# Kernel optimization log

Hardware: AMD Instinct MI355X
Metric: run time of the kernel (lower is better)

The kernel has to match this reference:

```python
import jax, jax.numpy as jnp
import numpy as np
import math

B, S, P, G = 8, 512, 64, 64
E, GE = 768, 32          # sub_embed_dim, gene_embed_dim
HD = E // 2              # sub_head_dim = 384
L = P * G
LAMBDA_INIT = 0.8 - 0.6 * math.exp(-0.3 * 0)  # depth=0 -> 0.2
SCALING = HD ** -0.5


def setup_inputs() -> dict:
    key0 = jax.random.key(0)
    ks = jax.random.split(key0, 12)
    init = 0.02
    return {
        "query": jax.random.normal(ks[0], (B, S, E), jnp.float32),
        "key": jax.random.normal(ks[1], (B, P, G, GE), jnp.float32),
        "query_mask": jax.random.bernoulli(ks[2], 0.9, (B, S)),
        "key_mask": jax.random.bernoulli(ks[3], 0.9, (B, P, G)),
        # weights stored [in, out] so y = x @ W (equiv to torch Linear no-bias)
        "Wq": jax.random.normal(ks[4], (E, E), jnp.float32) * init,
        "Wkv": jax.random.normal(ks[5], (GE, 2 * E), jnp.float32) * init,
        "Wout": jax.random.normal(ks[6], (E, E), jnp.float32) * init,
        "lambda_q1": jax.random.normal(ks[7], (HD,), jnp.float32) * 0.1,
        "lambda_k1": jax.random.normal(ks[8], (HD,), jnp.float32) * 0.1,
        "lambda_q2": jax.random.normal(ks[9], (HD,), jnp.float32) * 0.1,
        "lambda_k2": jax.random.normal(ks[10], (HD,), jnp.float32) * 0.1,
        "ln_weight": jnp.ones((E,), jnp.float32),  # RMSNorm affine weight (2*HD = E)
    }


def reference(query, key, query_mask, key_mask, Wq, Wkv, Wout,
              lambda_q1, lambda_k1, lambda_q2, lambda_k2, ln_weight):
    # Projections
    Q = query @ Wq                                   # [B,S,E]
    KV = key.reshape(B, L, GE) @ Wkv                 # [B,L,2E]
    K = KV[..., :E]                                  # [B,L,E]
    V = KV[..., E:]                                  # [B,L,E] (= 2*HD)

    # Split into 2 heads of dim HD
    Qh = Q.reshape(B, S, 2, HD).transpose(0, 2, 1, 3) * SCALING   # [B,2,S,HD]
    Kh = K.reshape(B, L, 2, HD).transpose(0, 2, 1, 3)             # [B,2,L,HD]

    # Combined mask [B,S,L]
    mask = query_mask[:, :, None] & key_mask.reshape(B, L)[:, None, :]

    # Dual attention scores + stable softmax (eps=1e-8 on denominator)
    scores = jnp.einsum('bhsd,bhld->bhsl', Qh, Kh)                # [B,2,S,L]
    scores = jnp.where(mask[:, None], scores, -1e20)
    m = jnp.max(scores, axis=-1, keepdims=True)
    p = jnp.exp(scores - m)
    attn = p / (jnp.sum(p, axis=-1, keepdims=True) + 1e-8)

    # Differential combination
    lam = (jnp.exp(jnp.sum(lambda_q1 * lambda_k1))
           - jnp.exp(jnp.sum(lambda_q2 * lambda_k2)) + LAMBDA_INIT)
    diff = attn[:, 0] - lam * attn[:, 1]                          # [B,S,L]
    diff = diff - jnp.min(diff, axis=-1, keepdims=True) + 1e-20
    diff = jnp.where(mask, diff, 0.0)

    # Value contraction: [B,S,L] @ [B,L,E] -> [B,S,E]
    attn_out = jnp.einsum('bsl,ble->bse', diff, V)

    # RMSNorm (eps=1e-5, affine) then scale by (1 - lambda_init)
    ms = jnp.mean(attn_out * attn_out, axis=-1, keepdims=True)
    attn_out = attn_out * jax.lax.rsqrt(ms + 1e-5) * ln_weight
    attn_out = attn_out * (1.0 - LAMBDA_INIT)

    out = attn_out @ Wout                                         # [B,S,E]
    return out, diff.reshape(B, S, P, G)
```

## Files before the change

kernel.cpp:

```cpp
#include <hip/hip_runtime.h>
#include <math.h>

#define LAM_INIT 0.2f
#define ONE_MINUS_LAM 0.8f
#define SCALING_F 0.05103103630798288f

typedef _Float16 h2 __attribute__((ext_vector_type(2)));

#if defined(__has_builtin)
#if __has_builtin(__builtin_amdgcn_fdot2)
#define FDOT2(a, b, c) __builtin_amdgcn_fdot2((a), (b), (c), false)
#endif
#endif
#ifndef FDOT2
#define FDOT2(a, b, c) ((float)(a).x * (float)(b).x + ((float)(a).y * (float)(b).y + (c)))
#endif

__device__ inline float waveMin(float v) {
#pragma unroll
    for (int o = 32; o > 0; o >>= 1) v = fminf(v, __shfl_xor(v, o));
    return v;
}
__device__ inline float waveSum(float v) {
#pragma unroll
    for (int o = 32; o > 0; o >>= 1) v += __shfl_xor(v, o);
    return v;
}

__global__ __launch_bounds__(256) void k01_prep(
    const float* __restrict__ key, const float* __restrict__ Wq,
    const float* __restrict__ Wkv, const float* __restrict__ Wout,
    const float* __restrict__ lq1, const float* __restrict__ lk1,
    const float* __restrict__ lq2, const float* __restrict__ lk2,
    const float* __restrict__ ln,
    unsigned* __restrict__ keyThU, float* __restrict__ Wcp,
    float* __restrict__ Wvp, float* __restrict__ lam,
    float* __restrict__ M)
{
    int blk = blockIdx.x;
    int tid = threadIdx.x;
    if (blk < 128) {
        int b  = blk >> 4;
        int l0 = (blk & 15) << 8;
        __shared__ float tile[256 * 33];
        const float* kp = key + ((size_t)b * 4096 + l0) * 32;
#pragma unroll
        for (int q = 0; q < 32; ++q) {
            int idx = tid + (q << 8);
            int r = idx >> 5, g = idx & 31;
            tile[r * 33 + g] = kp[idx];
        }
        __syncthreads();
#pragma unroll
        for (int gp = 0; gp < 16; ++gp) {
            h2 v;
            v.x = (_Float16)tile[tid * 33 + 2 * gp];
            v.y = (_Float16)tile[tid * 33 + 2 * gp + 1];
            keyThU[((size_t)(b * 16 + gp)) * 4096 + l0 + tid] =
                __builtin_bit_cast(unsigned, v);
        }
    } else if (blk < 512) {
        int bb = blk - 128;
        int kc = bb & 1;
        int ob = bb >> 1;
        int idx = ob * 256 + tid;
        int e  = idx >> 6;
        int hg = idx & 63;
        int h = hg >> 5, g = hg & 31;
        const float4* wqr = (const float4*)(Wq  + (size_t)e * 768 + h * 384 + kc * 192);
        const float4* wkr = (const float4*)(Wkv + (size_t)g * 1536 + h * 384 + kc * 192);
        float s0 = 0.f, s1 = 0.f;
#pragma unroll 4
        for (int d = 0; d < 48; d += 2) {
            float4 a0 = wqr[d],   b0 = wkr[d];
            float4 a1 = wqr[d+1], b1 = wkr[d+1];
            s0 += a0.x*b0.x + a0.y*b0.y + a0.z*b0.z + a0.w*b0.w;
            s1 += a1.x*b1.x + a1.y*b1.y + a1.z*b1.z + a1.w*b1.w;
        }
        Wcp[kc * 49152 + idx] = (s0 + s1) * SCALING_F;
    } else if (blk < 1280) {
        int bb = blk - 512;
        int kc = bb / 96;
        int ob = bb - kc * 96;
        int idx = ob * 256 + tid;
        int g = idx / 768;
        int e = idx - g * 768;
        const float* wvr = Wkv + (size_t)g * 1536 + 768;
        int c0 = kc * 96;
        float s0 = 0.f, s1 = 0.f;
#pragma unroll 4
        for (int c = c0; c < c0 + 96; c += 2) {
            s0 += wvr[c]   * ln[c]   * Wout[(size_t)c * 768 + e];
            s1 += wvr[c+1] * ln[c+1] * Wout[(size_t)(c+1) * 768 + e];
        }
        Wvp[kc * 24576 + idx] = s0 + s1;
    } else if (blk == 1280) {
        float s1 = 0.f, s2 = 0.f;
        for (int d = tid; d < 384; d += 256) {
            s1 += lq1[d] * lk1[d];
            s2 += lq2[d] * lk2[d];
        }
        s1 = waveSum(s1);
        s2 = waveSum(s2);
        __shared__ float r1[4], r2[4];
        int wid = tid >> 6, lane = tid & 63;
        if (lane == 0) { r1[wid] = s1; r2[wid] = s2; }
        __syncthreads();
        if (tid == 0) {
            float a  = r1[0] + r1[1] + r1[2] + r1[3];
            float b2 = r2[0] + r2[1] + r2[2] + r2[3];
            lam[0] = expf(a) - expf(b2) + LAM_INIT;
        }
    } else {
        int idx = (blk - 1281) * 256 + tid;
        int g = idx >> 5, gp = idx & 31;
        const float4* ra = (const float4*)(Wkv + (size_t)g  * 1536 + 768);
        const float4* rb = (const float4*)(Wkv + (size_t)gp * 1536 + 768);
        float s = 0.f;
#pragma unroll 4
        for (int q = 0; q < 192; ++q) {
            float4 a = ra[q], b = rb[q];
            s += a.x*b.x + a.y*b.y + a.z*b.z + a.w*b.w;
        }
        M[idx] = s;
    }
}

__global__ __launch_bounds__(256) void k2_qt(
    const float* __restrict__ query, const float* __restrict__ Wcp,
    const float* __restrict__ Wvp, float* __restrict__ WvoT,
    float* __restrict__ Qtp)
{
    int blk = blockIdx.x;
    int tid = threadIdx.x;
    if (blk >= 512) {
        int idx = (blk - 512) * 256 + tid;
        float s = 0.f;
#pragma unroll
        for (int kc = 0; kc < 8; ++kc) s += Wvp[kc * 24576 + idx];
        int g = idx / 768;
        int e = idx - g * 768;
        WvoT[(size_t)e * 32 + g] = s;
        return;
    }
    int kc = blk >> 7;
    int mt = blk & 127;
    int m0 = mt * 32;
    __shared__ __align__(16) float As[64 * 33];
    __shared__ __align__(16) float Bs[64 * 64];

    int tm = tid >> 5;
    int tn = tid & 31;
    float acc[4][2];
#pragma unroll
    for (int r = 0; r < 4; ++r) { acc[r][0] = 0.f; acc[r][1] = 0.f; }

    for (int ch = 0; ch < 3; ++ch) {
        int k0 = kc * 192 + ch * 64;
        __syncthreads();
#pragma unroll
        for (int q = 0; q < 2; ++q) {
            int f = tid + q * 256;
            int m = f >> 4, kq = f & 15;
            float4 v = *(const float4*)&query[(size_t)(m0 + m) * 768 + k0 + kq * 4];
            As[(kq * 4 + 0) * 33 + m] = v.x;
            As[(kq * 4 + 1) * 33 + m] = v.y;
            As[(kq * 4 + 2) * 33 + m] = v.z;
            As[(kq * 4 + 3) * 33 + m] = v.w;
        }
#pragma unroll
        for (int q = 0; q < 4; ++q) {
            int f = tid + q * 256;
            int kk = f >> 4, n4 = f & 15;
            float4 a = *(const float4*)&Wcp[(size_t)(k0 + kk) * 64 + n4 * 4];
            float4 b = *(const float4*)&Wcp[49152 + (size_t)(k0 + kk) * 64 + n4 * 4];
            float4 s; s.x = a.x + b.x; s.y = a.y + b.y; s.z = a.z + b.z; s.w = a.w + b.w;
            *(float4*)&Bs[kk * 64 + n4 * 4] = s;
        }
        __syncthreads();
#pragma unroll 8
        for (int kk = 0; kk < 64; ++kk) {
            float4 a = *(const float4*)&As[kk * 33 + tm * 4];
            float2 b = *(const float2*)&Bs[kk * 64 + tn * 2];
            acc[0][0] += a.x * b.x; acc[0][1] += a.x * b.y;
            acc[1][0] += a.y * b.x; acc[1][1] += a.y * b.y;
            acc[2][0] += a.z * b.x; acc[2][1] += a.z * b.y;
            acc[3][0] += a.w * b.x; acc[3][1] += a.w * b.y;
        }
    }
#pragma unroll
    for (int r = 0; r < 4; ++r) {
        float2 o; o.x = acc[r][0]; o.y = acc[r][1];
        *(float2*)&Qtp[(size_t)kc * 262144 + (size_t)(m0 + tm * 4 + r) * 64 + tn * 2] = o;
    }
}

__global__ __launch_bounds__(512, 4) void k3_attn(
    const float* __restrict__ Qtp, const unsigned* __restrict__ keyThU,
    const int* __restrict__ qmask, const int* __restrict__ kmask,
    const float* __restrict__ lamp, float* __restrict__ diffO)
{
    int blk = blockIdx.x;
    int b  = blk >> 7;
    int s0 = (blk & 127) * 4;
    int tid = threadIdx.x;
    int lane = tid & 63, wid = tid >> 6;

    __shared__ __align__(16) unsigned qt_th[128];
    __shared__ float redS[64];
    __shared__ float redM[32];

    if (tid < 128) {
        int ts = tid >> 5;
        int h  = (tid >> 4) & 1;
        int gp = tid & 15;
        size_t row = (size_t)(b * 512 + s0 + ts) * 64;
        int col = h * 32 + 2 * gp;
        float v0 = 0.f, v1 = 0.f;
#pragma unroll
        for (int kc = 0; kc < 4; ++kc) {
            v0 += Qtp[(size_t)kc * 262144 + row + col];
            v1 += Qtp[(size_t)kc * 262144 + row + col + 1];
        }
        h2 hv; hv.x = (_Float16)v0; hv.y = (_Float16)v1;
        qt_th[gp * 8 + ts * 2 + h] = __builtin_bit_cast(unsigned, hv);
    }
    int qm[4];
#pragma unroll
    for (int ts = 0; ts < 4; ++ts) qm[ts] = qmask[b * 512 + s0 + ts];
    float lam = lamp[0];

    unsigned kmb = 0;
#pragma unroll
    for (int c = 0; c < 2; ++c) {
        int4 km = *(const int4*)(kmask + b * 4096 + c * 2048 + tid * 4);
        if (km.x) kmb |= 1u << (c * 4 + 0);
        if (km.y) kmb |= 1u << (c * 4 + 1);
        if (km.z) kmb |= 1u << (c * 4 + 2);
        if (km.w) kmb |= 1u << (c * 4 + 3);
    }
    __syncthreads();

    float p[2][4][8];
#pragma unroll
    for (int h = 0; h < 2; ++h)
#pragma unroll
        for (int ts = 0; ts < 4; ++ts)
#pragma unroll
            for (int i = 0; i < 8; ++i) p[h][ts][i] = 0.f;

    const unsigned* kt = keyThU + (size_t)b * 16 * 4096 + tid * 4;
    for (int gp = 0; gp < 16; ++gp) {
        uint4 q0 = *(const uint4*)&qt_th[gp * 8];
        uint4 q1 = *(const uint4*)&qt_th[gp * 8 + 4];
        h2 qv[8];
        qv[0] = __builtin_bit_cast(h2, q0.x); qv[1] = __builtin_bit_cast(h2, q0.y);
        qv[2] = __builtin_bit_cast(h2, q0.z); qv[3] = __builtin_bit_cast(h2, q0.w);
        qv[4] = __builtin_bit_cast(h2, q1.x); qv[5] = __builtin_bit_cast(h2, q1.y);
        qv[6] = __builtin_bit_cast(h2, q1.z); qv[7] = __builtin_bit_cast(h2, q1.w);
        const unsigned* kg = kt + (size_t)gp * 4096;
#pragma unroll
        for (int c = 0; c < 2; ++c) {
            uint4 kv = *(const uint4*)(kg + c * 2048);
            h2 k0 = __builtin_bit_cast(h2, kv.x);
            h2 k1 = __builtin_bit_cast(h2, kv.y);
            h2 k2 = __builtin_bit_cast(h2, kv.z);
            h2 k3 = __builtin_bit_cast(h2, kv.w);
#pragma unroll
            for (int ts = 0; ts < 4; ++ts)
#pragma unroll
                for (int h = 0; h < 2; ++h) {
                    h2 q = qv[ts * 2 + h];
                    p[h][ts][c*4+0] = FDOT2(k0, q, p[h][ts][c*4+0]);
                    p[h][ts][c*4+1] = FDOT2(k1, q, p[h][ts][c*4+1]);
                    p[h][ts][c*4+2] = FDOT2(k2, q, p[h][ts][c*4+2]);
                    p[h][ts][c*4+3] = FDOT2(k3, q, p[h][ts][c*4+3]);
                }
        }
    }

    float inv[2][4];
#pragma unroll
    for (int h = 0; h < 2; ++h)
#pragma unroll
        for (int ts = 0; ts < 4; ++ts) {
            float s = 0.f;
#pragma unroll
            for (int i = 0; i < 8; ++i) {
                bool ok = qm[ts] && ((kmb >> i) & 1u);
                float e = ok ? __expf(p[h][ts][i]) : 0.f;
                p[h][ts][i] = e;
                s += e;
            }
            s = waveSum(s);
            if (lane == 0) redS[(h * 4 + ts) * 8 + wid] = s;
        }
    __syncthreads();
#pragma unroll
    for (int h = 0; h < 2; ++h)
#pragma unroll
        for (int ts = 0; ts < 4; ++ts) {
            int r = (h * 4 + ts) * 8;
            float s = redS[r];
#pragma unroll
            for (int w = 1; w < 8; ++w) s += redS[r + w];
            inv[h][ts] = 1.0f / (s + 1e-8f);
        }

    float mn[4];
#pragma unroll
    for (int ts = 0; ts < 4; ++ts) {
        float v = 3.4e38f;
#pragma unroll
        for (int i = 0; i < 8; ++i) {
            float d = p[0][ts][i] * inv[0][ts] - lam * (p[1][ts][i] * inv[1][ts]);
            p[0][ts][i] = d;
            v = fminf(v, d);
        }
        v = waveMin(v);
        if (lane == 0) redM[ts * 8 + wid] = v;
    }
    __syncthreads();
#pragma unroll
    for (int ts = 0; ts < 4; ++ts) {
        int r = ts * 8;
        float v = redM[r];
#pragma unroll
        for (int w = 1; w < 8; ++w) v = fminf(v, redM[r + w]);
        mn[ts] = v;
    }

#pragma unroll
    for (int ts = 0; ts < 4; ++ts) {
        size_t base = (size_t)(b * 512 + s0 + ts) * 4096 + tid * 4;
#pragma unroll
        for (int c = 0; c < 2; ++c) {
            float4 o;
            float v0 = p[0][ts][c*4+0] - mn[ts] + 1e-20f;
            float v1 = p[0][ts][c*4+1] - mn[ts] + 1e-20f;
            float v2 = p[0][ts][c*4+2] - mn[ts] + 1e-20f;
            float v3 = p[0][ts][c*4+3] - mn[ts] + 1e-20f;
            o.x = (qm[ts] && ((kmb >> (c*4+0)) & 1u)) ? v0 : 0.f;
            o.y = (qm[ts] && ((kmb >> (c*4+1)) & 1u)) ? v1 : 0.f;
            o.z = (qm[ts] && ((kmb >> (c*4+2)) & 1u)) ? v2 : 0.f;
            o.w = (qm[ts] && ((kmb >> (c*4+3)) & 1u)) ? v3 : 0.f;
            *(float4*)(diffO + base + c * 2048) = o;
        }
    }
}

__global__ __launch_bounds__(256) void k4_T(
    const float* __restrict__ diff, const float* __restrict__ key,
    float* __restrict__ P)
{
    int blk = blockIdx.x;
    int rt = blk & 63, kc = blk >> 6;
    int row0 = rt << 6;
    int b = row0 >> 9;
    int l0 = kc << 9;
    int tid = threadIdx.x;
    int tx = tid & 7;
    int ty = tid >> 3;
    int g0 = tx * 4;

    __shared__ __align__(16) float Ks[256][32];

    float acc[2][4];
#pragma unroll
    for (int r = 0; r < 2; ++r)
#pragma unroll
        for (int c2 = 0; c2 < 4; ++c2) acc[r][c2] = 0.f;

    for (int ph = 0; ph < 2; ++ph) {
        int lp = l0 + ph * 256;
        __syncthreads();
#pragma unroll
        for (int q = 0; q < 32; ++q) {
            int idx = tid + (q << 8);
            int r = idx >> 5, g = idx & 31;
            Ks[r][g] = key[((size_t)(b * 4096 + lp + r)) * 32 + g];
        }
        __syncthreads();

        for (int j4 = 0; j4 < 64; ++j4) {
            int l = lp + j4 * 4;
            float4 dv[2];
#pragma unroll
            for (int r = 0; r < 2; ++r)
                dv[r] = *(const float4*)(diff + (size_t)(row0 + ty * 2 + r) * 4096 + l);
#pragma unroll
            for (int jj = 0; jj < 4; ++jj) {
                float4 kq = *(const float4*)&Ks[j4 * 4 + jj][g0];
#pragma unroll
                for (int r = 0; r < 2; ++r) {
                    float d = (jj == 0) ? dv[r].x : (jj == 1) ? dv[r].y : (jj == 2) ? dv[r].z : dv[r].w;
                    acc[r][0] += d * kq.x;
                    acc[r][1] += d * kq.y;
                    acc[r][2] += d * kq.z;
                    acc[r][3] += d * kq.w;
                }
            }
        }
    }
#pragma unroll
    for (int r = 0; r < 2; ++r) {
        float4 o; o.x = acc[r][0]; o.y = acc[r][1]; o.z = acc[r][2]; o.w = acc[r][3];
        *(float4*)&P[(size_t)kc * 131072 + (size_t)(row0 + ty * 2 + r) * 32 + g0] = o;
    }
}

__global__ __launch_bounds__(256, 4) void k5_out(
    const float* __restrict__ P, const float* __restrict__ M,
    const float* __restrict__ WvoT, float* __restrict__ out)
{
    int row0 = blockIdx.x * 4;
    int tid = threadIdx.x;
    int w = tid >> 6;
    int lane = tid & 63;
    __shared__ __align__(16) float Ts[4][32];
    __shared__ __align__(16) float Ml[1024];

    if (tid < 128) {
        int r = tid >> 5, g = tid & 31;
        float s = 0.f;
#pragma unroll
        for (int kc = 0; kc < 8; ++kc)
            s += P[(size_t)kc * 131072 + (size_t)(row0 + r) * 32 + g];
        Ts[r][g] = s;
    }
#pragma unroll
    for (int q = 0; q < 4; ++q) Ml[tid + q * 256] = M[tid + q * 256];
    __syncthreads();

    float4 t[8];
#pragma unroll
    for (int q = 0; q < 8; ++q) t[q] = *(const float4*)&Ts[w][q * 4];

    float ssq = 0.f;
#pragma unroll
    for (int i = 0; i < 16; ++i) {
        int gg = lane + i * 64;
        int g = gg >> 5, gp = gg & 31;
        ssq = fmaf(Ts[w][g] * Ts[w][gp], Ml[gg], ssq);
    }
    ssq = waveSum(ssq);
    float rs = rsqrtf(ssq * (1.0f / 768.0f) + 1e-5f) * ONE_MINUS_LAM;

#pragma unroll
    for (int j = 0; j < 3; ++j) {
        int e0 = lane * 4 + j * 256;
        const float4* wp = (const float4*)(WvoT + (size_t)e0 * 32);
        float4 o; o.x = 0.f; o.y = 0.f; o.z = 0.f; o.w = 0.f;
#pragma unroll
        for (int q = 0; q < 8; ++q) {
            float4 a0 = wp[q];
            float4 a1 = wp[q + 8];
            float4 a2 = wp[q + 16];
            float4 a3 = wp[q + 24];
            o.x += t[q].x*a0.x + t[q].y*a0.y + t[q].z*a0.z + t[q].w*a0.w;
            o.y += t[q].x*a1.x + t[q].y*a1.y + t[q].z*a1.z + t[q].w*a1.w;
            o.z += t[q].x*a2.x + t[q].y*a2.y + t[q].z*a2.z + t[q].w*a2.w;
            o.w += t[q].x*a3.x + t[q].y*a3.y + t[q].z*a3.z + t[q].w*a3.w;
        }
        o.x *= rs; o.y *= rs; o.z *= rs; o.w *= rs;
        *(float4*)(out + (size_t)(row0 + w) * 768 + e0) = o;
    }
}

extern "C" void kernel_launch(void* const* d_in, const int* in_sizes, int n_in,
                              void* d_out, int out_size, void* d_ws, size_t ws_size,
                              hipStream_t stream) {
    (void)in_sizes; (void)n_in; (void)out_size; (void)ws_size;
    const float* query = (const float*)d_in[0];
    const float* key   = (const float*)d_in[1];
    const int*   qmask = (const int*)d_in[2];
    const int*   kmask = (const int*)d_in[3];
    const float* Wq    = (const float*)d_in[4];
    const float* Wkv   = (const float*)d_in[5];
    const float* Wout  = (const float*)d_in[6];
    const float* lq1   = (const float*)d_in[7];
    const float* lk1   = (const float*)d_in[8];
    const float* lq2   = (const float*)d_in[9];
    const float* lk2   = (const float*)d_in[10];
    const float* ln    = (const float*)d_in[11];

    float* out  = (float*)d_out;
    float* diff = out + 3145728;

    float* ws      = (float*)d_ws;
    float* Wcp     = ws;
    float* WvoT    = ws + 98304;
    float* Wvp     = ws + 122880;
    float* lam     = ws + 319488;
    unsigned* keyThU = (unsigned*)(ws + 319552);
    float* Qtp     = ws + 843840;
    float* P       = Qtp;
    float* Mbuf    = ws + 1892416;

    k01_prep<<<1285, 256, 0, stream>>>(key, Wq, Wkv, Wout, lq1, lk1, lq2, lk2, ln,
                                       keyThU, Wcp, Wvp, lam, Mbuf);
    k2_qt<<<608, 256, 0, stream>>>(query, Wcp, Wvp, WvoT, Qtp);
    k3_attn<<<1024, 512, 0, stream>>>(Qtp, keyThU, qmask, kmask, lam, diff);
    k4_T<<<512, 256, 0, stream>>>(diff, key, P);
    k5_out<<<1024, 256, 0, stream>>>(P, Mbuf, WvoT, out);
}
```

Measured before the change: 275.9 us.

## Fuse diff·key contraction with RMSNorm and output projection into one kernel

Merges the split-L partial contraction kernel and the output kernel into a single kernel. Each block owns 8 rows, loops over all 4096 L positions in 16 chunks, and reduces partials in shared memory instead of writing them to a global workspace. The RMSNorm sum of squares and the WvoT projection then run in the same block. This removes one launch and the global partial round-trip, but each block now walks the whole L dimension serially, which gives less parallelism per row.

```diff
diff --git a/kernel.cpp b/kernel.cpp
--- a/kernel.cpp
+++ b/kernel.cpp
@@ -349,121 +349,123 @@
     }
 }
 
-__global__ __launch_bounds__(256) void k4_T(
+__global__ __launch_bounds__(256) void k4_out(
     const float* __restrict__ diff, const float* __restrict__ key,
-    float* __restrict__ P)
+    const float* __restrict__ M, const float* __restrict__ WvoT,
+    float* __restrict__ out)
 {
-    int blk = blockIdx.x;
-    int rt = blk & 63, kc = blk >> 6;
-    int row0 = rt << 6;
+    int row0 = blockIdx.x * 8;
     int b = row0 >> 9;
-    int l0 = kc << 9;
     int tid = threadIdx.x;
-    int tx = tid & 7;
-    int ty = tid >> 3;
-    int g0 = tx * 4;
+    int lq = tid >> 5;
+    int rp = (tid >> 3) & 3;
+    int gq = tid & 7;
+    int g0 = gq * 4;
 
     __shared__ __align__(16) float Ks[256][32];
+    __shared__ __align__(16) float Tp[8][8][32];
+    __shared__ __align__(16) float Ml[1024];
+    __shared__ __align__(16) float Ts[8][32];
+    __shared__ float rs_s[8];
+
+#pragma unroll
+    for (int q = 0; q < 4; ++q) Ml[tid + q * 256] = M[tid + q * 256];
 
     float acc[2][4];
 #pragma unroll
     for (int r = 0; r < 2; ++r)
 #pragma unroll
-        for (int c2 = 0; c2 < 4; ++c2) acc[r][c2] = 0.f;
-
-    for (int ph = 0; ph < 2; ++ph) {
-        int lp = l0 + ph * 256;
+        for (int c = 0; c < 4; ++c) acc[r][c] = 0.f;
+
+    const float* d0 = diff + (size_t)(row0 + rp * 2 + 0) * 4096;
+    const float* d1 = diff + (size_t)(row0 + rp * 2 + 1) * 4096;
+
+    for (int ch = 0; ch < 16; ++ch) {
+        int lbase = ch * 256;
         __syncthreads();
 #pragma unroll
-        for (int q = 0; q < 32; ++q) {
-            int idx = tid + (q << 8);
-            int r = idx >> 5, g = idx & 31;
-            Ks[r][g] = key[((size_t)(b * 4096 + lp + r)) * 32 + g];
+        for (int q = 0; q < 8; ++q) {
+            int f = tid + q * 256;
+            int rr = f >> 3, g4 = f & 7;
+            *(float4*)&Ks[rr][g4 * 4] =
+                *(const float4*)&key[((size_t)(b * 4096 + lbase + rr)) * 32 + g4 * 4];
         }
         __syncthreads();
 
-        for (int j4 = 0; j4 < 64; ++j4) {
-            int l = lp + j4 * 4;
-            float4 dv[2];
-#pragma unroll
-            for (int r = 0; r < 2; ++r)
-                dv[r] = *(const float4*)(diff + (size_t)(row0 + ty * 2 + r) * 4096 + l);
-#pragma unroll
-            for (int jj = 0; jj < 4; ++jj) {
-                float4 kq = *(const float4*)&Ks[j4 * 4 + jj][g0];
-#pragma unroll
-                for (int r = 0; r < 2; ++r) {
-                    float d = (jj == 0) ? dv[r].x : (jj == 1) ? dv[r].y : (jj == 2) ? dv[r].z : dv[r].w;
-                    acc[r][0] += d * kq.x;
-                    acc[r][1] += d * kq.y;
-                    acc[r][2] += d * kq.z;
-                    acc[r][3] += d * kq.w;
-                }
+        int l0 = lbase + lq * 32;
+#pragma unroll 2
+        for (int j4 = 0; j4 < 8; ++j4) {
+            int l = l0 + j4 * 4;
+            float4 dv0 = *(const float4*)(d0 + l);
+            float4 dv1 = *(const float4*)(d1 + l);
+            int ll = lq * 32 + j4 * 4;
+#pragma unroll
+            for (int c = 0; c < 4; ++c) {
+                float4 kq = *(const float4*)&Ks[ll + c][g0];
+                float a = (c == 0) ? dv0.x : (c == 1) ? dv0.y : (c == 2) ? dv0.z : dv0.w;
+                float bq = (c == 0) ? dv1.x : (c == 1) ? dv1.y : (c == 2) ? dv1.z : dv1.w;
+                acc[0][0] += a * kq.x;  acc[0][1] += a * kq.y;
+                acc[0][2] += a * kq.z;  acc[0][3] += a * kq.w;
+                acc[1][0] += bq * kq.x; acc[1][1] += bq * kq.y;
+                acc[1][2] += bq * kq.z; acc[1][3] += bq * kq.w;
             }
         }
     }
-#pragma unroll
-    for (int r = 0; r < 2; ++r) {
-        float4 o; o.x = acc[r][0]; o.y = acc[r][1]; o.z = acc[r][2]; o.w = acc[r][3];
-        *(float4*)&P[(size_t)kc * 131072 + (size_t)(row0 + ty * 2 + r) * 32 + g0] = o;
-    }
-}
-
-__global__ __launch_bounds__(256, 4) void k5_out(
-    const float* __restrict__ P, const float* __restrict__ M,
-    const float* __restrict__ WvoT, float* __restrict__ out)
-{
-    int row0 = blockIdx.x * 4;
-    int tid = threadIdx.x;
-    int w = tid >> 6;
-    int lane = tid & 63;
-    __shared__ __align__(16) float Ts[4][32];
-    __shared__ __align__(16) float Ml[1024];
-
-    if (tid < 128) {
+
+    {
+        float4 o0; o0.x = acc[0][0]; o0.y = acc[0][1]; o0.z = acc[0][2]; o0.w = acc[0][3];
+        float4 o1; o1.x = acc[1][0]; o1.y = acc[1][1]; o1.z = acc[1][2]; o1.w = acc[1][3];
+        *(float4*)&Tp[lq][rp * 2 + 0][g0] = o0;
+        *(float4*)&Tp[lq][rp * 2 + 1][g0] = o1;
+    }
+    __syncthreads();
+    {
         int r = tid >> 5, g = tid & 31;
         float s = 0.f;
 #pragma unroll
-        for (int kc = 0; kc < 8; ++kc)
-            s += P[(size_t)kc * 131072 + (size_t)(row0 + r) * 32 + g];
+        for (int q = 0; q < 8; ++q) s += Tp[q][r][g];
         Ts[r][g] = s;
     }
-#pragma unroll
-    for (int q = 0; q < 4; ++q) Ml[tid + q * 256] = M[tid + q * 256];
     __syncthreads();
 
-    float4 t[8];
-#pragma unroll
-    for (int q = 0; q < 8; ++q) t[q] = *(const float4*)&Ts[w][q * 4];
-
-    float ssq = 0.f;
-#pragma unroll
-    for (int i = 0; i < 16; ++i) {
-        int gg = lane + i * 64;
-        int g = gg >> 5, gp = gg & 31;
-        ssq = fmaf(Ts[w][g] * Ts[w][gp], Ml[gg], ssq);
-    }
-    ssq = waveSum(ssq);
-    float rs = rsqrtf(ssq * (1.0f / 768.0f) + 1e-5f) * ONE_MINUS_LAM;
-
-#pragma unroll
-    for (int j = 0; j < 3; ++j) {
-        int e0 = lane * 4 + j * 256;
-        const float4* wp = (const float4*)(WvoT + (size_t)e0 * 32);
-        float4 o; o.x = 0.f; o.y = 0.f; o.z = 0.f; o.w = 0.f;
-#pragma unroll
-        for (int q = 0; q < 8; ++q) {
-            float4 a0 = wp[q];
-            float4 a1 = wp[q + 8];
-            float4 a2 = wp[q + 16];
-            float4 a3 = wp[q + 24];
-            o.x += t[q].x*a0.x + t[q].y*a0.y + t[q].z*a0.z + t[q].w*a0.w;
-            o.y += t[q].x*a1.x + t[q].y*a1.y + t[q].z*a1.z + t[q].w*a1.w;
-            o.z += t[q].x*a2.x + t[q].y*a2.y + t[q].z*a2.z + t[q].w*a2.w;
-            o.w += t[q].x*a3.x + t[q].y*a3.y + t[q].z*a3.z + t[q].w*a3.w;
-        }
-        o.x *= rs; o.y *= rs; o.z *= rs; o.w *= rs;
-        *(float4*)(out + (size_t)(row0 + w) * 768 + e0) = o;
+    {
+        int r = tid >> 5, gp = tid & 31;
+        float inner = 0.f;
+#pragma unroll
+        for (int g = 0; g < 32; ++g) inner = fmaf(Ts[r][g], Ml[g * 32 + gp], inner);
+        float part = inner * Ts[r][gp];
+#pragma unroll
+        for (int o = 16; o > 0; o >>= 1) part += __shfl_xor(part, o);
+        if (gp == 0)
+            rs_s[r] = rsqrtf(part * (1.0f / 768.0f) + 1e-5f) * ONE_MINUS_LAM;
+    }
+    __syncthreads();
+
+    {
+        int r = tid >> 5, c0 = tid & 31;
+        float rs = rs_s[r];
+        float4 t[8];
+#pragma unroll
+        for (int q = 0; q < 8; ++q) t[q] = *(const float4*)&Ts[r][q * 4];
+#pragma unroll
+        for (int j = 0; j < 6; ++j) {
+            int e = c0 * 4 + j * 128;
+            const float4* wp = (const float4*)(WvoT + (size_t)e * 32);
+            float4 o; o.x = 0.f; o.y = 0.f; o.z = 0.f; o.w = 0.f;
+#pragma unroll
+            for (int q = 0; q < 8; ++q) {
+                float4 a0 = wp[q];
+                float4 a1 = wp[q + 8];
+                float4 a2 = wp[q + 16];
+                float4 a3 = wp[q + 24];
+                o.x += t[q].x*a0.x + t[q].y*a0.y + t[q].z*a0.z + t[q].w*a0.w;
+                o.y += t[q].x*a1.x + t[q].y*a1.y + t[q].z*a1.z + t[q].w*a1.w;
+                o.z += t[q].x*a2.x + t[q].y*a2.y + t[q].z*a2.z + t[q].w*a2.w;
+                o.w += t[q].x*a3.x + t[q].y*a3.y + t[q].z*a3.z + t[q].w*a3.w;
+            }
+            o.x *= rs; o.y *= rs; o.z *= rs; o.w *= rs;
+            *(float4*)(out + (size_t)(row0 + r) * 768 + e) = o;
+        }
     }
 }
 
@@ -494,13 +496,11 @@
     float* lam     = ws + 319488;
     unsigned* keyThU = (unsigned*)(ws + 319552);
     float* Qtp     = ws + 843840;
-    float* P       = Qtp;
     float* Mbuf    = ws + 1892416;
 
     k01_prep<<<1285, 256, 0, stream>>>(key, Wq, Wkv, Wout, lq1, lk1, lq2, lk2, ln,
                                        keyThU, Wcp, Wvp, lam, Mbuf);
     k2_qt<<<608, 256, 0, stream>>>(query, Wcp, Wvp, WvoT, Qtp);
     k3_attn<<<1024, 512, 0, stream>>>(Qtp, keyThU, qmask, kmask, lam, diff);
-    k4_T<<<512, 256, 0, stream>>>(diff, key, P);
-    k5_out<<<1024, 256, 0, stream>>>(P, Mbuf, WvoT, out);
-}
+    k4_out<<<512, 256, 0, stream>>>(diff, key, Mbuf, WvoT, out);
+}
```

Measured after the change: 275.1 us. No clear change (-0.3%).
